# Kernel optimization log

Measured on AMD Instinct MI355X. Metric: run time of the kernel, lower is better.

## Reference

```python
import jax, jax.numpy as jnp
import numpy as np

B, P, E, S = 4, 2048, 4096, 16


def setup_inputs() -> dict:
    key = jax.random.key(0)
    ks = jax.random.split(key, 6)
    return {
        "x": jax.random.normal(ks[0], (B, P, E), dtype=jnp.float32),
        "product": jax.random.normal(ks[1], (P, S), dtype=jnp.float32) * 0.1,
        "person": jax.random.normal(ks[2], (E, S), dtype=jnp.float32) * 0.1,
        "W1": jax.random.normal(ks[3], (2 * S, S), dtype=jnp.float32) * (1.0 / np.sqrt(2 * S)),
        "W2": jax.random.normal(ks[4], (S, S), dtype=jnp.float32) * (1.0 / np.sqrt(S)),
        "W3": jax.random.normal(ks[5], (S, 1), dtype=jnp.float32) * (1.0 / np.sqrt(S)),
    }


def reference(x, product, person, W1, W2, W3):
    # cartesian product concat([pr, pe]) @ W1 == pr @ W1[:S] + pe @ W1[S:]
    # (no bias), so we avoid materializing the (P*E, 2S) concat tensor.
    Wa, Wb = W1[:S], W1[S:]           # each (S, S)
    h1 = jnp.tanh(
        (product @ Wa)[:, None, :] +  # (P, 1, S)
        (person @ Wb)[None, :, :]     # (1, E, S)
    )                                  # (P, E, S)
    h2 = jnp.tanh(h1 @ W2)            # (P, E, S)
    z = (h2 @ W3)[..., 0]             # (P, E)
    score = jnp.where(z >= 0, z, 0.1 * z)  # leaky relu, alpha=0.1
    return score[None, :, :] * x      # (B, P, E)
```

## Files before the change

kernel.cpp:

```cpp
#include <hip/hip_runtime.h>

#define BB 4
#define PP 2048
#define EE 4096
#define SS 16
#define TP 16
#define EBLK 256

typedef __fp16 v2h __attribute__((ext_vector_type(2)));
typedef __fp16 v4h __attribute__((ext_vector_type(4)));
typedef float  v4f __attribute__((ext_vector_type(4)));

static __device__ __forceinline__ float fast_tanh(float x) {
    float xc = fminf(fmaxf(x, -9.0f), 9.0f);
    float t  = __builtin_amdgcn_exp2f(xc * 2.885390081777927f);
    return (t - 1.0f) * __builtin_amdgcn_rcpf(t + 1.0f);
}

__global__ __launch_bounds__(256) void precompute_ab(
    const float* __restrict__ product, const float* __restrict__ person,
    const float* __restrict__ W1, float* __restrict__ a, float* __restrict__ b)
{
    int row = blockIdx.x * blockDim.x + threadIdx.x;
    if (row >= PP + EE) return;
    const bool  is_p  = row < PP;
    const float* in   = is_p ? (product + (size_t)row * SS)
                             : (person  + (size_t)(row - PP) * SS);
    const float* W    = is_p ? W1 : (W1 + SS * SS);
    float*       orow = is_p ? (a + (size_t)row * SS)
                             : (b + (size_t)(row - PP) * SS);
    float v[SS];
#pragma unroll
    for (int k = 0; k < SS; ++k) v[k] = in[k];
#pragma unroll
    for (int j = 0; j < SS; ++j) {
        float acc = 0.0f;
#pragma unroll
        for (int k = 0; k < SS; ++k) acc = fmaf(v[k], W[k * SS + j], acc);
        orow[j] = acc;
    }
}

__global__ __launch_bounds__(256, 4) void score_mul(
    const float* __restrict__ x, const float* __restrict__ a,
    const float* __restrict__ b, const float* __restrict__ W2,
    const float* __restrict__ W3, float* __restrict__ out)
{
    const int tid  = threadIdx.x;
    const int lane = tid & 63;
    const int wv   = tid >> 6;
    const int n    = lane & 15;
    const int q    = lane >> 4;

    const int e  = blockIdx.x * EBLK + tid;
    const int p0 = blockIdx.y * TP;

    __shared__ int h1s[4][64][8];

    float br[SS];
    {
        const float4* brp = (const float4*)(b + (size_t)e * SS);
#pragma unroll
        for (int i = 0; i < 4; ++i) {
            float4 t = brp[i];
            br[4*i+0]=t.x; br[4*i+1]=t.y; br[4*i+2]=t.z; br[4*i+3]=t.w;
        }
    }

    v4h w2a;
    {
        float c0 = W2[(q*4+0)*SS + n];
        float c1 = W2[(q*4+1)*SS + n];
        float c2 = W2[(q*4+2)*SS + n];
        float c3 = W2[(q*4+3)*SS + n];
        v2h lo = __builtin_amdgcn_cvt_pkrtz(c0, c1);
        v2h hi = __builtin_amdgcn_cvt_pkrtz(c2, c3);
        w2a[0]=lo[0]; w2a[1]=lo[1]; w2a[2]=hi[0]; w2a[3]=hi[1];
    }

    float4 w3v = ((const float4*)W3)[q];
    const float w3r[4] = {w3v.x, w3v.y, w3v.z, w3v.w};

    for (int ip = 0; ip < TP; ++ip) {
        const int p = p0 + ip;
        const size_t base = (size_t)p * EE + (size_t)e;

        float xv[BB];
#pragma unroll
        for (int bb2 = 0; bb2 < BB; ++bb2)
            xv[bb2] = x[(size_t)bb2 * ((size_t)PP * EE) + base];

        const float* __restrict__ ap = a + (size_t)p * SS;
        int hp[8];
#pragma unroll
        for (int r = 0; r < 8; ++r) {
            float t0 = fast_tanh(ap[2*r+0] + br[2*r+0]);
            float t1 = fast_tanh(ap[2*r+1] + br[2*r+1]);
            hp[r] = __builtin_bit_cast(int, __builtin_amdgcn_cvt_pkrtz(t0, t1));
        }

        int* myrow = &h1s[wv][lane][0];
        *(int4*)(myrow + 0) = make_int4(hp[0], hp[1], hp[2], hp[3]);
        *(int4*)(myrow + 4) = make_int4(hp[4], hp[5], hp[6], hp[7]);
        __builtin_amdgcn_wave_barrier();

        v4f acc[4];
#pragma unroll
        for (int g = 0; g < 4; ++g) {
            int2 rb = *(const int2*)&h1s[wv][g*16 + n][q*2];
            v4h bfrag = __builtin_bit_cast(v4h, rb);
            v4f z4 = {0.f, 0.f, 0.f, 0.f};
            acc[g] = __builtin_amdgcn_mfma_f32_16x16x16f16(w2a, bfrag, z4, 0, 0, 0);
        }

        float pg[4];
#pragma unroll
        for (int g = 0; g < 4; ++g) {
            float s = 0.f;
#pragma unroll
            for (int r = 0; r < 4; ++r)
                s = fmaf(fast_tanh(acc[g][r]), w3r[r], s);
            s += __shfl_xor(s, 16);
            s += __shfl_xor(s, 32);
            pg[g] = s;
        }
        float s01 = (q & 1) ? pg[1] : pg[0];
        float s23 = (q & 1) ? pg[3] : pg[2];
        float z   = (q & 2) ? s23 : s01;
        float sc  = fmaxf(z, 0.f) + 0.1f * fminf(z, 0.f);

#pragma unroll
        for (int bb2 = 0; bb2 < BB; ++bb2)
            out[(size_t)bb2 * ((size_t)PP * EE) + base] = sc * xv[bb2];
    }
}

extern "C" void kernel_launch(void* const* d_in, const int* in_sizes, int n_in,
                              void* d_out, int out_size, void* d_ws, size_t ws_size,
                              hipStream_t stream)
{
    const float* x       = (const float*)d_in[0];
    const float* product = (const float*)d_in[1];
    const float* person  = (const float*)d_in[2];
    const float* W1      = (const float*)d_in[3];
    const float* W2      = (const float*)d_in[4];
    const float* W3      = (const float*)d_in[5];
    float* out = (float*)d_out;

    float* a = (float*)d_ws;
    float* b = a + (size_t)PP * SS;

    dim3 g1((PP + EE + 255) / 256);
    precompute_ab<<<g1, 256, 0, stream>>>(product, person, W1, a, b);

    dim3 g2(EE / EBLK, PP / TP);
    score_mul<<<g2, 256, 0, stream>>>(x, a, b, W2, W3, out);
}
```

Before: 266.8 us.

## Compute h1 directly in MFMA fragment layout, removing LDS staging

Each lane now loads the slice of b that matches its MFMA B-fragment position (four e rows, its q quarter of S), so it computes tanh(a+b) for exactly the fragment elements it needs. This removes the per-iteration LDS write, wave barrier and LDS read. It also cuts the tanh work per lane from 16 to the 16 fragment elements without redundancy, simplifies fast_tanh to 1-2/(t+1) without clamping, drops the occupancy hint and hoists pointer arithmetic. The risk is the unclamped tanh: exp2 overflow to inf still gives 1, so it should stay correct.

```diff
diff --git a/kernel.cpp b/kernel.cpp
--- a/kernel.cpp
+++ b/kernel.cpp
@@ -12,9 +12,8 @@
 typedef float  v4f __attribute__((ext_vector_type(4)));
 
 static __device__ __forceinline__ float fast_tanh(float x) {
-    float xc = fminf(fmaxf(x, -9.0f), 9.0f);
-    float t  = __builtin_amdgcn_exp2f(xc * 2.885390081777927f);
-    return (t - 1.0f) * __builtin_amdgcn_rcpf(t + 1.0f);
+    float t = __builtin_amdgcn_exp2f(x * 2.885390081777927f);
+    return fmaf(-2.0f, __builtin_amdgcn_rcpf(t + 1.0f), 1.0f);
 }
 
 __global__ __launch_bounds__(256) void precompute_ab(
@@ -41,85 +40,71 @@
     }
 }
 
-__global__ __launch_bounds__(256, 4) void score_mul(
+__global__ __launch_bounds__(256) void score_mul(
     const float* __restrict__ x, const float* __restrict__ a,
     const float* __restrict__ b, const float* __restrict__ W2,
     const float* __restrict__ W3, float* __restrict__ out)
 {
     const int tid  = threadIdx.x;
     const int lane = tid & 63;
-    const int wv   = tid >> 6;
     const int n    = lane & 15;
     const int q    = lane >> 4;
 
-    const int e  = blockIdx.x * EBLK + tid;
+    const int eown = blockIdx.x * EBLK + tid;
+    const int ebase = blockIdx.x * EBLK + (tid & ~63);
     const int p0 = blockIdx.y * TP;
 
-    __shared__ int h1s[4][64][8];
-
-    float br[SS];
-    {
-        const float4* brp = (const float4*)(b + (size_t)e * SS);
+    float4 brg[4];
 #pragma unroll
-        for (int i = 0; i < 4; ++i) {
-            float4 t = brp[i];
-            br[4*i+0]=t.x; br[4*i+1]=t.y; br[4*i+2]=t.z; br[4*i+3]=t.w;
-        }
-    }
+    for (int g = 0; g < 4; ++g)
+        brg[g] = *(const float4*)(b + (size_t)(ebase + g*16 + n) * SS + q*4);
 
     v4h w2a;
     {
-        float c0 = W2[(q*4+0)*SS + n];
-        float c1 = W2[(q*4+1)*SS + n];
-        float c2 = W2[(q*4+2)*SS + n];
-        float c3 = W2[(q*4+3)*SS + n];
-        v2h lo = __builtin_amdgcn_cvt_pkrtz(c0, c1);
-        v2h hi = __builtin_amdgcn_cvt_pkrtz(c2, c3);
+        v2h lo = __builtin_amdgcn_cvt_pkrtz(W2[(q*4+0)*SS + n], W2[(q*4+1)*SS + n]);
+        v2h hi = __builtin_amdgcn_cvt_pkrtz(W2[(q*4+2)*SS + n], W2[(q*4+3)*SS + n]);
         w2a[0]=lo[0]; w2a[1]=lo[1]; w2a[2]=hi[0]; w2a[3]=hi[1];
     }
 
     float4 w3v = ((const float4*)W3)[q];
     const float w3r[4] = {w3v.x, w3v.y, w3v.z, w3v.w};
 
+    size_t base0 = (size_t)p0 * EE + (size_t)eown;
+    const float* __restrict__ xp0 = x   + base0;
+    float*       __restrict__ op0 = out + base0;
+
     for (int ip = 0; ip < TP; ++ip) {
         const int p = p0 + ip;
-        const size_t base = (size_t)p * EE + (size_t)e;
+        const size_t off = (size_t)ip * EE;
 
         float xv[BB];
 #pragma unroll
         for (int bb2 = 0; bb2 < BB; ++bb2)
-            xv[bb2] = x[(size_t)bb2 * ((size_t)PP * EE) + base];
+            xv[bb2] = xp0[(size_t)bb2 * ((size_t)PP * EE) + off];
 
-        const float* __restrict__ ap = a + (size_t)p * SS;
-        int hp[8];
-#pragma unroll
-        for (int r = 0; r < 8; ++r) {
-            float t0 = fast_tanh(ap[2*r+0] + br[2*r+0]);
-            float t1 = fast_tanh(ap[2*r+1] + br[2*r+1]);
-            hp[r] = __builtin_bit_cast(int, __builtin_amdgcn_cvt_pkrtz(t0, t1));
-        }
+        float4 av = *(const float4*)(a + (size_t)p * SS + q*4);
 
-        int* myrow = &h1s[wv][lane][0];
-        *(int4*)(myrow + 0) = make_int4(hp[0], hp[1], hp[2], hp[3]);
-        *(int4*)(myrow + 4) = make_int4(hp[4], hp[5], hp[6], hp[7]);
-        __builtin_amdgcn_wave_barrier();
-
-        v4f acc[4];
+        v4h bfrag[4];
 #pragma unroll
         for (int g = 0; g < 4; ++g) {
-            int2 rb = *(const int2*)&h1s[wv][g*16 + n][q*2];
-            v4h bfrag = __builtin_bit_cast(v4h, rb);
-            v4f z4 = {0.f, 0.f, 0.f, 0.f};
-            acc[g] = __builtin_amdgcn_mfma_f32_16x16x16f16(w2a, bfrag, z4, 0, 0, 0);
+            float t0 = fast_tanh(av.x + brg[g].x);
+            float t1 = fast_tanh(av.y + brg[g].y);
+            float t2 = fast_tanh(av.z + brg[g].z);
+            float t3 = fast_tanh(av.w + brg[g].w);
+            v2h lo = __builtin_amdgcn_cvt_pkrtz(t0, t1);
+            v2h hi = __builtin_amdgcn_cvt_pkrtz(t2, t3);
+            bfrag[g][0]=lo[0]; bfrag[g][1]=lo[1]; bfrag[g][2]=hi[0]; bfrag[g][3]=hi[1];
         }
 
         float pg[4];
 #pragma unroll
         for (int g = 0; g < 4; ++g) {
+            v4f z4 = {0.f, 0.f, 0.f, 0.f};
+            v4f acc = __builtin_amdgcn_mfma_f32_16x16x16f16(w2a, bfrag[g], z4, 0, 0, 0);
             float s = 0.f;
 #pragma unroll
             for (int r = 0; r < 4; ++r)
-                s = fmaf(fast_tanh(acc[g][r]), w3r[r], s);
+                s = fmaf(fast_tanh(acc[r]), w3r[r], s);
             s += __shfl_xor(s, 16);
             s += __shfl_xor(s, 32);
             pg[g] = s;
@@ -131,7 +116,7 @@
 
 #pragma unroll
         for (int bb2 = 0; bb2 < BB; ++bb2)
-            out[(size_t)bb2 * ((size_t)PP * EE) + base] = sc * xv[bb2];
+            op0[(size_t)bb2 * ((size_t)PP * EE) + off] = sc * xv[bb2];
     }
 }
 
```

After: 266.4 us. No clear change (-0.1%).
